# Optimization experiments

Measured on AMD Instinct MI355X. Metric: run time of the kernel, lower is better.

Reference implementation:

```python
import jax, jax.numpy as jnp
import numpy as np

HID = 256
HEADS = 8
HEAD_DIM = HID // HEADS

def setup_inputs() -> dict:
    key = jax.random.key(0)
    ks = jax.random.split(key, 12)
    B, S = 2, 4096
    scale = 1.0 / np.sqrt(HID)
    inp = {
        "query": jax.random.normal(ks[0], (B, S, HID), jnp.float32),
        "key": jax.random.normal(ks[1], (B, S, HID), jnp.float32),
        "value": jax.random.normal(ks[2], (B, S, HID), jnp.float32),
        "mask": jax.random.randint(ks[3], (B, 1, S), 0, 2, jnp.int32),
        "Wq": jax.random.normal(ks[4], (HID, HID), jnp.float32) * scale,
        "bq": jnp.zeros((HID,), jnp.float32),
        "Wk": jax.random.normal(ks[5], (HID, HID), jnp.float32) * scale,
        "bk": jnp.zeros((HID,), jnp.float32),
        "Wv": jax.random.normal(ks[6], (HID, HID), jnp.float32) * scale,
        "bv": jnp.zeros((HID,), jnp.float32),
        "Wo": jax.random.normal(ks[7], (HID, HID), jnp.float32) * scale,
        "bo": jnp.zeros((HID,), jnp.float32),
    }
    return inp

def reference(query, key, value, mask, Wq, bq, Wk, bk, Wv, bv, Wo, bo):
    B, Sq, _ = query.shape
    Sk = key.shape[1]
    # QKV projections, split into heads: [B, H, S, Dh]
    q = (query @ Wq + bq).reshape(B, Sq, HEADS, HEAD_DIM).transpose(0, 2, 1, 3)
    k = (key @ Wk + bk).reshape(B, Sk, HEADS, HEAD_DIM).transpose(0, 2, 1, 3)
    v = (value @ Wv + bv).reshape(B, Sk, HEADS, HEAD_DIM).transpose(0, 2, 1, 3)
    scores = jnp.einsum('bhqd,bhkd->bhqk', q, k) / jnp.sqrt(jnp.float32(HEAD_DIM))
    # mask [B,1,Sk] -> unsqueeze head dim -> [B,1,1,Sk], masked_fill(mask==0, -inf)
    m = mask[:, None, :, :]
    scores = jnp.where(m == 0, -jnp.inf, scores)
    attn = jax.nn.softmax(scores, axis=-1)  # dropout p=0.0 -> identity
    weighted = jnp.einsum('bhqk,bhkd->bhqd', attn, v)
    weighted = weighted.transpose(0, 2, 1, 3).reshape(B, Sq, HID)
    return weighted @ Wo + bo
```

## Files before the change

### kernel.cpp

```cpp
#include <hip/hip_runtime.h>
#include <math.h>

#define HID   256
#define HEADS 8
#define DH    32
#define BATCH 2
#define SEQ   4096
#define NTOK  (BATCH*SEQ)

typedef float f32x4 __attribute__((ext_vector_type(4)));
typedef short s16x8 __attribute__((ext_vector_type(8)));
typedef short s16x4 __attribute__((ext_vector_type(4)));
typedef unsigned int u32x2 __attribute__((ext_vector_type(2)));

__device__ __forceinline__ unsigned short bf16_rne(float f) {
  unsigned u = __float_as_uint(f);
  unsigned r = u + 0x7fffu + ((u >> 16) & 1u);
  return (unsigned short)(r >> 16);
}

__device__ __forceinline__ s16x8 cvt_bf16x8(f32x4 a, f32x4 b) {
  s16x8 t;
  t[0] = (short)bf16_rne(a[0]); t[1] = (short)bf16_rne(a[1]);
  t[2] = (short)bf16_rne(a[2]); t[3] = (short)bf16_rne(a[3]);
  t[4] = (short)bf16_rne(b[0]); t[5] = (short)bf16_rne(b[1]);
  t[6] = (short)bf16_rne(b[2]); t[7] = (short)bf16_rne(b[3]);
  return t;
}

__global__ __launch_bounds__(256) void prep_kernel(
    const float* __restrict__ Wq, const float* __restrict__ Wk,
    const float* __restrict__ Wv, const float* __restrict__ Wo,
    const int* __restrict__ mask,
    unsigned short* __restrict__ wT,
    unsigned short* __restrict__ mbf, float qscale)
{
  int id = blockIdx.x * 256 + threadIdx.x;
  if (id < 4 * 65536) {
    int w = id >> 16;
    int r = id & 65535;
    int n = r >> 8, k = r & 255;
    const float* W = (w == 0) ? Wq : (w == 1) ? Wk : (w == 2) ? Wv : Wo;
    float v = W[k * 256 + n];
    if (w == 0) v *= qscale;
    wT[id] = bf16_rne(v);
  } else if (id < 4 * 65536 + NTOK) {
    int i = id - 4 * 65536;
    mbf[i] = mask[i] ? (unsigned short)0x3F80 : (unsigned short)0;
  }
}

__global__ __launch_bounds__(256) void qkv_proj(
    const float* __restrict__ qin, const float* __restrict__ kin,
    const float* __restrict__ vin, const int* __restrict__ mask,
    const unsigned short* __restrict__ wT,
    const float* __restrict__ bq, const float* __restrict__ bk,
    const float* __restrict__ bv,
    unsigned short* __restrict__ q_ws, unsigned short* __restrict__ kh_ws,
    unsigned short* __restrict__ vt_ws, float qscale)
{
  __shared__ unsigned short As[2][64 * 40];
  __shared__ unsigned short Ws[2][64 * 40];

  const int z = blockIdx.z;
  const float* A = (z == 0) ? qin : (z == 1) ? kin : vin;
  const unsigned short* W = wT + z * 65536;
  const float* bias = (z == 0) ? bq : (z == 1) ? bk : bv;
  const float bscale = (z == 0) ? qscale : 1.f;

  const int tid = threadIdx.x;
  const int lane = tid & 63;
  const int wv = tid >> 6;
  const int l16 = lane & 15, q4 = lane >> 4;
  const int Mblk = blockIdx.x * 64, Nblk = blockIdx.y * 64;
  const int M0 = Mblk + (wv & 1) * 32;
  const int N0 = Nblk + (wv >> 1) * 32;

  const int srow = tid >> 2, scol = (tid & 3) * 8;
  const float* Aps = A + (size_t)(Mblk + srow) * 256 + scol;
  const unsigned short* Wps = W + (size_t)(Nblk + srow) * 256 + scol;
  unsigned short* adst = &As[0][srow * 40 + scol];
  unsigned short* wdst = &Ws[0][srow * 40 + scol];

  f32x4 areg0, areg1; s16x8 wreg;

#define LOADCH(K) do {                                                         \
    areg0 = *(const f32x4*)(Aps + (K) * 32);                                   \
    areg1 = *(const f32x4*)(Aps + (K) * 32 + 4);                               \
    wreg  = *(const s16x8*)(Wps + (K) * 32);                                   \
  } while (0)
#define WRITECH(B) do {                                                        \
    *(s16x8*)(adst + (B) * (64 * 40)) = cvt_bf16x8(areg0, areg1);              \
    *(s16x8*)(wdst + (B) * (64 * 40)) = wreg;                                  \
  } while (0)

  f32x4 acc[2][2] = {};

  LOADCH(0); WRITECH(0); LOADCH(1);
  for (int k = 0; k < 8; ++k) {
    __syncthreads();
    if (k + 1 < 8) WRITECH((k + 1) & 1);
    if (k + 2 < 8) LOADCH(k + 2);
    const unsigned short* AL = &As[k & 1][0];
    const unsigned short* WL = &Ws[k & 1][0];
    s16x8 af[2], wf[2];
#pragma unroll
    for (int i = 0; i < 2; ++i)
      af[i] = *(const s16x8*)(AL + ((wv & 1) * 32 + i * 16 + l16) * 40 + q4 * 8);
#pragma unroll
    for (int j = 0; j < 2; ++j)
      wf[j] = *(const s16x8*)(WL + ((wv >> 1) * 32 + j * 16 + l16) * 40 + q4 * 8);
#pragma unroll
    for (int i = 0; i < 2; ++i)
#pragma unroll
      for (int j = 0; j < 2; ++j)
        acc[i][j] = __builtin_amdgcn_mfma_f32_16x16x32_bf16(af[i], wf[j], acc[i][j], 0, 0, 0);
  }
#undef LOADCH
#undef WRITECH

#pragma unroll
  for (int j = 0; j < 2; ++j) {
    int n = N0 + j * 16 + l16;
    float bb = bias[n] * bscale;
#pragma unroll
    for (int i = 0; i < 2; ++i) {
      int m0 = M0 + i * 16 + q4 * 4;
      f32x4 c = acc[i][j];
      c[0] += bb; c[1] += bb; c[2] += bb; c[3] += bb;
      if (z == 0) {
#pragma unroll
        for (int r = 0; r < 4; ++r)
          q_ws[(size_t)(m0 + r) * 256 + n] = bf16_rne(c[r]);
      } else if (z == 1) {
        int bi = m0 >> 12, s = m0 & 4095;
        int h = n >> 5, d = n & 31;
        unsigned short* o = kh_ws + ((size_t)(bi * 8 + h) * 4096 + s) * 32 + d;
#pragma unroll
        for (int r = 0; r < 4; ++r) o[(size_t)r * 32] = bf16_rne(c[r]);
      } else {
#pragma unroll
        for (int r = 0; r < 4; ++r) c[r] *= (float)mask[m0 + r];
        int bi = m0 >> 12, s = m0 & 4095;
        int h = n >> 5, d = n & 31;
        int T = s >> 6, sl = s & 63;
        unsigned lo = (unsigned)bf16_rne(c[0]) | ((unsigned)bf16_rne(c[1]) << 16);
        unsigned hi = (unsigned)bf16_rne(c[2]) | ((unsigned)bf16_rne(c[3]) << 16);
        unsigned* dst = (unsigned*)(vt_ws +
            ((size_t)((bi * 8 + h) * 64 + T) * 32 + d) * 64 + sl);
        dst[0] = lo; dst[1] = hi;
      }
    }
  }
}

__global__ __launch_bounds__(256, 7) void flash_kernel(
    const unsigned short* __restrict__ q_ws, const unsigned short* __restrict__ kh_ws,
    const unsigned short* __restrict__ vt_ws, const unsigned short* __restrict__ mbf,
    float* __restrict__ pO, float* __restrict__ pL)
{
  __shared__ unsigned short Kb[2][64 * 40];
  __shared__ unsigned short Vb[2][32 * 72];

  const int idx = blockIdx.x;
  const int qt = idx & 31;
  const int kq = (idx >> 5) & 3;
  const int bh = idx >> 7;
  const int b = bh >> 3, h = bh & 7;
  const int tid = threadIdx.x;
  const int lane = tid & 63;
  const int wv = tid >> 6;
  const int l16 = lane & 15, q4 = lane >> 4;
  const int q0 = qt * 128 + wv * 32;

  s16x8 Qf[2];
#pragma unroll
  for (int qh = 0; qh < 2; ++qh)
    Qf[qh] = *(const s16x8*)(q_ws +
        (size_t)(b * 4096 + q0 + qh * 16 + l16) * 256 + h * 32 + q4 * 8);

  const unsigned short* Ksrc = kh_ws + ((size_t)bh * 4096 + kq * 1024) * 32;
  const unsigned short* Vsrc = vt_ws + (size_t)bh * 64 * 2048 + (size_t)kq * 16 * 2048;
  const unsigned short* Msrc = mbf + b * 4096 + kq * 1024 + q4 * 4;

  unsigned short* kdst = &Kb[0][(tid >> 2) * 40 + (tid & 3) * 8];
  unsigned short* vdst = &Vb[0][(tid >> 3) * 72 + (tid & 7) * 8];

  f32x4 o[2][2] = {{{0.f,0.f,0.f,0.f},{0.f,0.f,0.f,0.f}},
                   {{0.f,0.f,0.f,0.f},{0.f,0.f,0.f,0.f}}};
  f32x4 l[2] = {{0.f,0.f,0.f,0.f},{0.f,0.f,0.f,0.f}};

  const unsigned sel = (l16 == 0) ? 0xFFFFFFFFu : 0u;

  s16x8 kreg, vreg;

#define STAGE_LOAD(T) do {                                                     \
    kreg = *(const s16x8*)(Ksrc + (size_t)(T) * 2048 + tid * 8);               \
    vreg = *(const s16x8*)(Vsrc + (size_t)(T) * 2048 + tid * 8);               \
  } while (0)
#define STAGE_WRITE(B) do {                                                    \
    *(s16x8*)(kdst + (B) * (64 * 40)) = kreg;                                  \
    *(s16x8*)(vdst + (B) * (32 * 72)) = vreg;                                  \
  } while (0)

#define COMPUTE(B, T) do {                                                     \
    const unsigned short* KL = &Kb[B][0];                                      \
    const unsigned short* VL = &Vb[B][0];                                      \
    const f32x4 zz = {0.f, 0.f, 0.f, 0.f};                                     \
    s16x4 mreg[4];                                                             \
    _Pragma("unroll") for (int t = 0; t < 4; ++t)                              \
      mreg[t] = *(const s16x4*)(Msrc + (T) * 64 + t * 16);                     \
    _Pragma("unroll") for (int t = 0; t < 4; ++t) {                            \
      s16x8 kf = *(const s16x8*)(KL + (t * 16 + l16) * 40 + q4 * 8);           \
      f32x4 sc0 = __builtin_amdgcn_mfma_f32_16x16x32_bf16(kf, Qf[0], zz, 0, 0, 0); \
      f32x4 sc1 = __builtin_amdgcn_mfma_f32_16x16x32_bf16(kf, Qf[1], zz, 0, 0, 0); \
      unsigned a0 = __float_as_uint(__builtin_amdgcn_exp2f(sc0[0])) + 0x8000u; \
      unsigned a1 = __float_as_uint(__builtin_amdgcn_exp2f(sc0[1])) + 0x8000u; \
      unsigned a2 = __float_as_uint(__builtin_amdgcn_exp2f(sc0[2])) + 0x8000u; \
      unsigned a3 = __float_as_uint(__builtin_amdgcn_exp2f(sc0[3])) + 0x8000u; \
      unsigned c0 = __float_as_uint(__builtin_amdgcn_exp2f(sc1[0])) + 0x8000u; \
      unsigned c1 = __float_as_uint(__builtin_amdgcn_exp2f(sc1[1])) + 0x8000u; \
      unsigned c2 = __float_as_uint(__builtin_amdgcn_exp2f(sc1[2])) + 0x8000u; \
      unsigned c3 = __float_as_uint(__builtin_amdgcn_exp2f(sc1[3])) + 0x8000u; \
      u32x2 pk0, pk1;                                                          \
      pk0[0] = __builtin_amdgcn_perm(a1, a0, 0x07060302u);                     \
      pk0[1] = __builtin_amdgcn_perm(a3, a2, 0x07060302u);                     \
      pk1[0] = __builtin_amdgcn_perm(c1, c0, 0x07060302u);                     \
      pk1[1] = __builtin_amdgcn_perm(c3, c2, 0x07060302u);                     \
      s16x4 pf0 = __builtin_bit_cast(s16x4, pk0);                              \
      s16x4 pf1 = __builtin_bit_cast(s16x4, pk1);                              \
      u32x2 mm = __builtin_bit_cast(u32x2, mreg[t]);                           \
      mm[0] &= sel; mm[1] &= sel;                                              \
      s16x4 onesb = __builtin_bit_cast(s16x4, mm);                             \
      s16x4 vf0 = *(const s16x4*)(VL + l16 * 72 + t * 16 + q4 * 4);            \
      s16x4 vf1 = *(const s16x4*)(VL + (l16 + 16) * 72 + t * 16 + q4 * 4);     \
      o[0][0] = __builtin_amdgcn_mfma_f32_16x16x16bf16_1k(pf0, vf0, o[0][0], 0, 0, 0); \
      o[0][1] = __builtin_amdgcn_mfma_f32_16x16x16bf16_1k(pf0, vf1, o[0][1], 0, 0, 0); \
      o[1][0] = __builtin_amdgcn_mfma_f32_16x16x16bf16_1k(pf1, vf0, o[1][0], 0, 0, 0); \
      o[1][1] = __builtin_amdgcn_mfma_f32_16x16x16bf16_1k(pf1, vf1, o[1][1], 0, 0, 0); \
      l[0] = __builtin_amdgcn_mfma_f32_16x16x16bf16_1k(pf0, onesb, l[0], 0, 0, 0); \
      l[1] = __builtin_amdgcn_mfma_f32_16x16x16bf16_1k(pf1, onesb, l[1], 0, 0, 0); \
    }                                                                          \
  } while (0)

  STAGE_LOAD(0); STAGE_WRITE(0);
  STAGE_LOAD(1);

  for (int T = 0; T < 16; ++T) {
    __syncthreads();
    if (T + 1 < 16) STAGE_WRITE((T + 1) & 1);
    if (T + 2 < 16) STAGE_LOAD(T + 2);
    COMPUTE(T & 1, T);
  }
#undef STAGE_LOAD
#undef STAGE_WRITE
#undef COMPUTE

  float* pob = pO + (((size_t)kq * 16 + bh) * 4096 + q0) * 32;
#pragma unroll
  for (int qh = 0; qh < 2; ++qh)
#pragma unroll
    for (int r = 0; r < 4; ++r) {
      int q = qh * 16 + q4 * 4 + r;
      pob[(size_t)q * 32 + l16]      = o[qh][0][r];
      pob[(size_t)q * 32 + l16 + 16] = o[qh][1][r];
    }
  if (l16 == 0) {
    float* plb = pL + ((size_t)kq * 16 + bh) * 4096 + q0;
#pragma unroll
    for (int qh = 0; qh < 2; ++qh)
#pragma unroll
      for (int r = 0; r < 4; ++r)
        plb[qh * 16 + q4 * 4 + r] = l[qh][r];
  }
}

__global__ __launch_bounds__(256) void combine_kernel(
    const float* __restrict__ pO, const float* __restrict__ pL,
    unsigned short* __restrict__ wtd)
{
  int id = blockIdx.x * 256 + threadIdx.x;
  int d4 = id & 7;
  int q  = (id >> 3) & 4095;
  int bh = id >> 15;
  int b = bh >> 3, h = bh & 7;
  const size_t OS = (size_t)16 * 4096 * 32;
  const size_t LS = (size_t)16 * 4096;
  size_t i0 = ((size_t)bh * 4096 + q) * 32 + d4 * 4;
  f32x4 s = *(const f32x4*)(pO + i0);
  float lt = pL[(size_t)bh * 4096 + q];
#pragma unroll
  for (int kq = 1; kq < 4; ++kq) {
    f32x4 c = *(const f32x4*)(pO + kq * OS + i0);
    s[0] += c[0]; s[1] += c[1]; s[2] += c[2]; s[3] += c[3];
    lt += pL[kq * LS + (size_t)bh * 4096 + q];
  }
  float inv = 1.0f / lt;
  unsigned lo = (unsigned)bf16_rne(s[0] * inv) | ((unsigned)bf16_rne(s[1] * inv) << 16);
  unsigned hi = (unsigned)bf16_rne(s[2] * inv) | ((unsigned)bf16_rne(s[3] * inv) << 16);
  unsigned* dst = (unsigned*)(wtd + ((size_t)(b * 4096 + q) * 256) + h * 32 + d4 * 4);
  dst[0] = lo; dst[1] = hi;
}

__global__ __launch_bounds__(256) void o_proj(
    const unsigned short* __restrict__ wtd, const unsigned short* __restrict__ woT,
    const float* __restrict__ bo, float* __restrict__ out)
{
  const int lane = threadIdx.x & 63;
  const int wv = threadIdx.x >> 6;
  const int l16 = lane & 15, q4 = lane >> 4;
  const int M0 = blockIdx.x * 64 + (wv & 1) * 32;
  const int N0 = blockIdx.y * 64 + (wv >> 1) * 32;

  f32x4 acc[2][2] = {};
  for (int k0 = 0; k0 < 256; k0 += 32) {
    s16x8 af[2], wf[2];
#pragma unroll
    for (int i = 0; i < 2; ++i)
      af[i] = *(const s16x8*)(wtd + (size_t)(M0 + i * 16 + l16) * 256 + k0 + q4 * 8);
#pragma unroll
    for (int j = 0; j < 2; ++j)
      wf[j] = *(const s16x8*)(woT + (size_t)(N0 + j * 16 + l16) * 256 + k0 + q4 * 8);
#pragma unroll
    for (int i = 0; i < 2; ++i)
#pragma unroll
      for (int j = 0; j < 2; ++j)
        acc[i][j] = __builtin_amdgcn_mfma_f32_16x16x32_bf16(af[i], wf[j], acc[i][j], 0, 0, 0);
  }

#pragma unroll
  for (int j = 0; j < 2; ++j) {
    int n = N0 + j * 16 + l16;
    float bb = bo[n];
#pragma unroll
    for (int i = 0; i < 2; ++i) {
      int m0 = M0 + i * 16 + q4 * 4;
#pragma unroll
      for (int r = 0; r < 4; ++r)
        out[(size_t)(m0 + r) * 256 + n] = acc[i][j][r] + bb;
    }
  }
}

extern "C" void kernel_launch(void* const* d_in, const int* in_sizes, int n_in,
                              void* d_out, int out_size, void* d_ws, size_t ws_size,
                              hipStream_t stream) {
  const float* query = (const float*)d_in[0];
  const float* key   = (const float*)d_in[1];
  const float* value = (const float*)d_in[2];
  const int*   mask  = (const int*)d_in[3];
  const float* Wq = (const float*)d_in[4];
  const float* bq = (const float*)d_in[5];
  const float* Wk = (const float*)d_in[6];
  const float* bk = (const float*)d_in[7];
  const float* Wv = (const float*)d_in[8];
  const float* bv = (const float*)d_in[9];
  const float* Wo = (const float*)d_in[10];
  const float* bo = (const float*)d_in[11];
  float* out = (float*)d_out;

  char* p = (char*)d_ws;
  unsigned short* q_ws  = (unsigned short*)p; p += (size_t)NTOK * HID * 2;
  unsigned short* kh_ws = (unsigned short*)p; p += (size_t)NTOK * HID * 2;
  unsigned short* vt_ws = (unsigned short*)p; p += (size_t)NTOK * HID * 2;
  unsigned short* wtd   = (unsigned short*)p; p += (size_t)NTOK * HID * 2;
  unsigned short* wT    = (unsigned short*)p; p += (size_t)4 * 65536 * 2;
  unsigned short* mbf   = (unsigned short*)p; p += (size_t)NTOK * 2;
  float* pO             = (float*)p;          p += (size_t)4 * 16 * 4096 * 32 * 4;
  float* pL             = (float*)p;          p += (size_t)4 * 16 * 4096 * 4;

  const float qscale = 1.0f / (sqrtf(32.0f) * logf(2.0f));

  prep_kernel<<<(4 * 65536 + NTOK + 255) / 256, 256, 0, stream>>>(
      Wq, Wk, Wv, Wo, mask, wT, mbf, qscale);
  qkv_proj<<<dim3(NTOK / 64, HID / 64, 3), 256, 0, stream>>>(
      query, key, value, mask, wT, bq, bk, bv, q_ws, kh_ws, vt_ws, qscale);
  flash_kernel<<<dim3(2048), 256, 0, stream>>>(
      q_ws, kh_ws, vt_ws, mbf, pO, pL);
  combine_kernel<<<dim3(2048), 256, 0, stream>>>(pO, pL, wtd);
  o_proj<<<dim3(NTOK / 64, HID / 64), 256, 0, stream>>>(
      wtd, wT + 3 * 65536, bo, out);
}
```

Baseline: 182.5 us.

## Halve flash key splits, permute LDS rows, shrink V padding, drop exp rounding bias

The flash kernel now splits the key range into 2 chunks instead of 4, so each block runs 32 key tiles. The grid halves to 1024 blocks, and the partial-output buffers and combine reduction shrink to match. This cuts partial-sum traffic and combine work in exchange for fewer blocks and longer serial loops. It also permutes the LDS row mapping for the K and QKV staging tiles, changes V padding from 72 to 68 with split 4-wide stores to reduce bank conflicts, and removes the +0x8000 rounding add on exp values before bf16 truncation, which slightly changes numerics.

```diff
diff --git a/kernel.cpp b/kernel.cpp
--- a/kernel.cpp
+++ b/kernel.cpp
@@ -26,6 +26,10 @@
   t[4] = (short)bf16_rne(b[0]); t[5] = (short)bf16_rne(b[1]);
   t[6] = (short)bf16_rne(b[2]); t[7] = (short)bf16_rne(b[3]);
   return t;
+}
+
+__device__ __forceinline__ int permrow(int idx) {
+  return (idx & ~15) | (idx & 8) | ((idx & 1) << 2) | ((idx >> 1) & 3);
 }
 
 __global__ __launch_bounds__(256) void prep_kernel(
@@ -76,7 +80,7 @@
   const int M0 = Mblk + (wv & 1) * 32;
   const int N0 = Nblk + (wv >> 1) * 32;
 
-  const int srow = tid >> 2, scol = (tid & 3) * 8;
+  const int srow = permrow(tid >> 2), scol = (tid & 3) * 8;
   const float* Aps = A + (size_t)(Mblk + srow) * 256 + scol;
   const unsigned short* Wps = W + (size_t)(Nblk + srow) * 256 + scol;
   unsigned short* adst = &As[0][srow * 40 + scol];
@@ -160,12 +164,12 @@
     float* __restrict__ pO, float* __restrict__ pL)
 {
   __shared__ unsigned short Kb[2][64 * 40];
-  __shared__ unsigned short Vb[2][32 * 72];
+  __shared__ unsigned short Vb[2][32 * 68];
 
   const int idx = blockIdx.x;
   const int qt = idx & 31;
-  const int kq = (idx >> 5) & 3;
-  const int bh = idx >> 7;
+  const int kq = (idx >> 5) & 1;
+  const int bh = idx >> 6;
   const int b = bh >> 3, h = bh & 7;
   const int tid = threadIdx.x;
   const int lane = tid & 63;
@@ -179,12 +183,14 @@
     Qf[qh] = *(const s16x8*)(q_ws +
         (size_t)(b * 4096 + q0 + qh * 16 + l16) * 256 + h * 32 + q4 * 8);
 
-  const unsigned short* Ksrc = kh_ws + ((size_t)bh * 4096 + kq * 1024) * 32;
-  const unsigned short* Vsrc = vt_ws + (size_t)bh * 64 * 2048 + (size_t)kq * 16 * 2048;
-  const unsigned short* Msrc = mbf + b * 4096 + kq * 1024 + q4 * 4;
-
-  unsigned short* kdst = &Kb[0][(tid >> 2) * 40 + (tid & 3) * 8];
-  unsigned short* vdst = &Vb[0][(tid >> 3) * 72 + (tid & 7) * 8];
+  const unsigned short* Ksrc = kh_ws + ((size_t)bh * 4096 + kq * 2048) * 32;
+  const unsigned short* Vsrc = vt_ws + (size_t)bh * 64 * 2048 + (size_t)kq * 32 * 2048;
+  const unsigned short* Msrc = mbf + b * 4096 + kq * 2048 + q4 * 4;
+
+  const int krow = permrow(tid >> 2), kcol = (tid & 3) * 8;
+  const unsigned short* kps = Ksrc + krow * 32 + kcol;
+  unsigned short* kdst = &Kb[0][krow * 40 + kcol];
+  unsigned short* vdst = &Vb[0][(tid >> 3) * 68 + (tid & 7) * 8];
 
   f32x4 o[2][2] = {{{0.f,0.f,0.f,0.f},{0.f,0.f,0.f,0.f}},
                    {{0.f,0.f,0.f,0.f},{0.f,0.f,0.f,0.f}}};
@@ -195,12 +201,15 @@
   s16x8 kreg, vreg;
 
 #define STAGE_LOAD(T) do {                                                     \
-    kreg = *(const s16x8*)(Ksrc + (size_t)(T) * 2048 + tid * 8);               \
+    kreg = *(const s16x8*)(kps + (size_t)(T) * 2048);                          \
     vreg = *(const s16x8*)(Vsrc + (size_t)(T) * 2048 + tid * 8);               \
   } while (0)
 #define STAGE_WRITE(B) do {                                                    \
     *(s16x8*)(kdst + (B) * (64 * 40)) = kreg;                                  \
-    *(s16x8*)(vdst + (B) * (32 * 72)) = vreg;                                  \
+    s16x4 _vlo = __builtin_shufflevector(vreg, vreg, 0, 1, 2, 3);              \
+    s16x4 _vhi = __builtin_shufflevector(vreg, vreg, 4, 5, 6, 7);              \
+    *(s16x4*)(vdst + (B) * (32 * 68)) = _vlo;                                  \
+    *(s16x4*)(vdst + (B) * (32 * 68) + 4) = _vhi;                              \
   } while (0)
 
 #define COMPUTE(B, T) do {                                                     \
@@ -214,14 +223,14 @@
       s16x8 kf = *(const s16x8*)(KL + (t * 16 + l16) * 40 + q4 * 8);           \
       f32x4 sc0 = __builtin_amdgcn_mfma_f32_16x16x32_bf16(kf, Qf[0], zz, 0, 0, 0); \
       f32x4 sc1 = __builtin_amdgcn_mfma_f32_16x16x32_bf16(kf, Qf[1], zz, 0, 0, 0); \
-      unsigned a0 = __float_as_uint(__builtin_amdgcn_exp2f(sc0[0])) + 0x8000u; \
-      unsigned a1 = __float_as_uint(__builtin_amdgcn_exp2f(sc0[1])) + 0x8000u; \
-      unsigned a2 = __float_as_uint(__builtin_amdgcn_exp2f(sc0[2])) + 0x8000u; \
-      unsigned a3 = __float_as_uint(__builtin_amdgcn_exp2f(sc0[3])) + 0x8000u; \
-      unsigned c0 = __float_as_uint(__builtin_amdgcn_exp2f(sc1[0])) + 0x8000u; \
-      unsigned c1 = __float_as_uint(__builtin_amdgcn_exp2f(sc1[1])) + 0x8000u; \
-      unsigned c2 = __float_as_uint(__builtin_amdgcn_exp2f(sc1[2])) + 0x8000u; \
-      unsigned c3 = __float_as_uint(__builtin_amdgcn_exp2f(sc1[3])) + 0x8000u; \
+      unsigned a0 = __float_as_uint(__builtin_amdgcn_exp2f(sc0[0]));           \
+      unsigned a1 = __float_as_uint(__builtin_amdgcn_exp2f(sc0[1]));           \
+      unsigned a2 = __float_as_uint(__builtin_amdgcn_exp2f(sc0[2]));           \
+      unsigned a3 = __float_as_uint(__builtin_amdgcn_exp2f(sc0[3]));           \
+      unsigned c0 = __float_as_uint(__builtin_amdgcn_exp2f(sc1[0]));           \
+      unsigned c1 = __float_as_uint(__builtin_amdgcn_exp2f(sc1[1]));           \
+      unsigned c2 = __float_as_uint(__builtin_amdgcn_exp2f(sc1[2]));           \
+      unsigned c3 = __float_as_uint(__builtin_amdgcn_exp2f(sc1[3]));           \
       u32x2 pk0, pk1;                                                          \
       pk0[0] = __builtin_amdgcn_perm(a1, a0, 0x07060302u);                     \
       pk0[1] = __builtin_amdgcn_perm(a3, a2, 0x07060302u);                     \
@@ -232,8 +241,8 @@
       u32x2 mm = __builtin_bit_cast(u32x2, mreg[t]);                           \
       mm[0] &= sel; mm[1] &= sel;                                              \
       s16x4 onesb = __builtin_bit_cast(s16x4, mm);                             \
-      s16x4 vf0 = *(const s16x4*)(VL + l16 * 72 + t * 16 + q4 * 4);            \
-      s16x4 vf1 = *(const s16x4*)(VL + (l16 + 16) * 72 + t * 16 + q4 * 4);     \
+      s16x4 vf0 = *(const s16x4*)(VL + l16 * 68 + t * 16 + q4 * 4);            \
+      s16x4 vf1 = *(const s16x4*)(VL + (l16 + 16) * 68 + t * 16 + q4 * 4);     \
       o[0][0] = __builtin_amdgcn_mfma_f32_16x16x16bf16_1k(pf0, vf0, o[0][0], 0, 0, 0); \
       o[0][1] = __builtin_amdgcn_mfma_f32_16x16x16bf16_1k(pf0, vf1, o[0][1], 0, 0, 0); \
       o[1][0] = __builtin_amdgcn_mfma_f32_16x16x16bf16_1k(pf1, vf0, o[1][0], 0, 0, 0); \
@@ -246,10 +255,10 @@
   STAGE_LOAD(0); STAGE_WRITE(0);
   STAGE_LOAD(1);
 
-  for (int T = 0; T < 16; ++T) {
+  for (int T = 0; T < 32; ++T) {
     __syncthreads();
-    if (T + 1 < 16) STAGE_WRITE((T + 1) & 1);
-    if (T + 2 < 16) STAGE_LOAD(T + 2);
+    if (T + 1 < 32) STAGE_WRITE((T + 1) & 1);
+    if (T + 2 < 32) STAGE_LOAD(T + 2);
     COMPUTE(T & 1, T);
   }
 #undef STAGE_LOAD
@@ -288,13 +297,9 @@
   const size_t LS = (size_t)16 * 4096;
   size_t i0 = ((size_t)bh * 4096 + q) * 32 + d4 * 4;
   f32x4 s = *(const f32x4*)(pO + i0);
-  float lt = pL[(size_t)bh * 4096 + q];
-#pragma unroll
-  for (int kq = 1; kq < 4; ++kq) {
-    f32x4 c = *(const f32x4*)(pO + kq * OS + i0);
-    s[0] += c[0]; s[1] += c[1]; s[2] += c[2]; s[3] += c[3];
-    lt += pL[kq * LS + (size_t)bh * 4096 + q];
-  }
+  f32x4 c = *(const f32x4*)(pO + OS + i0);
+  s[0] += c[0]; s[1] += c[1]; s[2] += c[2]; s[3] += c[3];
+  float lt = pL[(size_t)bh * 4096 + q] + pL[LS + (size_t)bh * 4096 + q];
   float inv = 1.0f / lt;
   unsigned lo = (unsigned)bf16_rne(s[0] * inv) | ((unsigned)bf16_rne(s[1] * inv) << 16);
   unsigned hi = (unsigned)bf16_rne(s[2] * inv) | ((unsigned)bf16_rne(s[3] * inv) << 16);
@@ -366,8 +371,8 @@
   unsigned short* wtd   = (unsigned short*)p; p += (size_t)NTOK * HID * 2;
   unsigned short* wT    = (unsigned short*)p; p += (size_t)4 * 65536 * 2;
   unsigned short* mbf   = (unsigned short*)p; p += (size_t)NTOK * 2;
-  float* pO             = (float*)p;          p += (size_t)4 * 16 * 4096 * 32 * 4;
-  float* pL             = (float*)p;          p += (size_t)4 * 16 * 4096 * 4;
+  float* pO             = (float*)p;          p += (size_t)2 * 16 * 4096 * 32 * 4;
+  float* pL             = (float*)p;          p += (size_t)2 * 16 * 4096 * 4;
 
   const float qscale = 1.0f / (sqrtf(32.0f) * logf(2.0f));
 
@@ -375,7 +380,7 @@
       Wq, Wk, Wv, Wo, mask, wT, mbf, qscale);
   qkv_proj<<<dim3(NTOK / 64, HID / 64, 3), 256, 0, stream>>>(
       query, key, value, mask, wT, bq, bk, bv, q_ws, kh_ws, vt_ws, qscale);
-  flash_kernel<<<dim3(2048), 256, 0, stream>>>(
+  flash_kernel<<<dim3(1024), 256, 0, stream>>>(
       q_ws, kh_ws, vt_ws, mbf, pO, pL);
   combine_kernel<<<dim3(2048), 256, 0, stream>>>(pO, pL, wtd);
   o_proj<<<dim3(NTOK / 64, HID / 64), 256, 0, stream>>>(
```

Result: slower. 199.1 us (+9.1%).
